# Optimization experiments

Hardware: AMD Instinct MI355X
Metric: run time of the kernel (lower is better)

## Reference

```python
import jax, jax.numpy as jnp
import numpy as np

M, K, N = 4096, 4096, 11008


def setup_inputs() -> dict:
    key = jax.random.key(0)
    k1, k2, k3 = jax.random.split(key, 3)
    x = jax.random.normal(k1, (M, K), dtype=jnp.float16)
    weight_packed = jax.random.randint(k2, ((K + 1) // 2, N), 0, 256, dtype=jnp.int32)
    weight_scale = jax.random.uniform(k3, (N,), dtype=jnp.float32) * 0.05 + 1e-3
    return {"x": x, "weight_packed": weight_packed, "weight_scale": weight_scale}


def reference(x, weight_packed, weight_scale):
    # Unpack int4 nibbles: low nibble -> even K index, high nibble -> odd K index.
    packed = weight_packed.astype(jnp.uint8)                      # [K//2, N]
    low = (packed & 15).astype(jnp.float32) - 8.0                 # even rows
    high = ((packed >> 4) & 15).astype(jnp.float32) - 8.0         # odd rows
    k = x.shape[-1]
    w = jnp.stack([low, high], axis=1).reshape(-1, low.shape[1])[:k]  # [K, N]
    # Per-output-feature symmetric scale, then fp16 GEMM (matches torch fallback).
    w = (w * weight_scale[None, :]).astype(jnp.float16)
    out = jnp.matmul(x, w)                                        # [M, N] fp16
    return out
```

## Files before the change

### kernel.cpp

```cpp
#include <hip/hip_runtime.h>
#include <hip/hip_fp16.h>
#include <stdint.h>


#define M_DIM 4096
#define K_DIM 4096
#define N_DIM 11008
#define KH    (K_DIM / 2)

#define WS_XH_BYTES  ((size_t)M_DIM * K_DIM * 2)

typedef __attribute__((ext_vector_type(8))) _Float16 f16x8;
typedef __attribute__((ext_vector_type(2))) _Float16 h2;
typedef __attribute__((ext_vector_type(4))) float f32x4;

__device__ __forceinline__ unsigned pack_f16_pair(float lo, float hi) {
    return __builtin_bit_cast(unsigned, __builtin_amdgcn_cvt_pkrtz(lo, hi));
}

__device__ __forceinline__ unsigned dq_pair(unsigned v) {
    unsigned c = (v & 0xFu) | ((v << 12) & 0x000F0000u) | 0x64006400u;
    h2 r = __builtin_bit_cast(h2, c) + __builtin_bit_cast(h2, 0xE408E408u);
    return __builtin_bit_cast(unsigned, r);
}

__device__ __forceinline__ void gld_lds16(const void* g, void* l) {
    __builtin_amdgcn_global_load_lds(
        (const __attribute__((address_space(1))) unsigned int*)g,
        (__attribute__((address_space(3))) unsigned int*)l,
        16, 0, 0);
}

__global__ void __launch_bounds__(256) cvt_x_kernel(
    const float* __restrict__ X, unsigned short* __restrict__ Xh)
{
    size_t i = ((size_t)blockIdx.x * 256 + threadIdx.x) * 8;
    float4 a = *(const float4*)(X + i);
    float4 b = *(const float4*)(X + i + 4);
    uint4 o = make_uint4(pack_f16_pair(a.x, a.y), pack_f16_pair(a.z, a.w),
                         pack_f16_pair(b.x, b.y), pack_f16_pair(b.z, b.w));
    *(uint4*)(Xh + i) = o;
}

__global__ void __launch_bounds__(256) dqt_kernel(
    const int* __restrict__ WP, unsigned* __restrict__ Wt)
{
    __shared__ unsigned Lt[64][65];
    const int t = threadIdx.x;
    const int n0 = blockIdx.x * 64;
    const int r0 = blockIdx.y * 64;
    const int g = t >> 6, l = t & 63;
#pragma unroll
    for (int i = 0; i < 16; ++i) {
        const int r = r0 + g * 16 + i;
        Lt[l][g * 16 + i] = dq_pair((unsigned)WP[(size_t)r * N_DIM + n0 + l]);
    }
    __syncthreads();
    const int nr = t >> 2, sg = t & 3;
    unsigned* dst = Wt + (size_t)(n0 + nr) * KH + r0 + sg * 16;
#pragma unroll
    for (int c = 0; c < 4; ++c) {
        uint4 v = make_uint4(Lt[nr][sg * 16 + c * 4 + 0], Lt[nr][sg * 16 + c * 4 + 1],
                             Lt[nr][sg * 16 + c * 4 + 2], Lt[nr][sg * 16 + c * 4 + 3]);
        *(uint4*)(dst + c * 4) = v;
    }
}

__global__ void __launch_bounds__(512, 2) qgemm9_kernel(
    const unsigned short* __restrict__ Xh,
    const unsigned*       __restrict__ Wt,
    const float*          __restrict__ WS,
    float*                __restrict__ Out)
{
    __shared__ unsigned short LA[2][2][8192];
    __shared__ unsigned short LB[2][2][8192];

    const int t = threadIdx.x;
    const int w = t >> 6;
    const int l = t & 63;

    const int bid = blockIdx.x;
    const int xcd = bid & 7;
    const int i8  = bid >> 3;
    const int bx  = i8 >> 1;
    const int by  = (xcd << 1) | (i8 & 1);
    const int bm0 = by * 256;
    const int bn0 = bx * 256;

    const int wr = w >> 2;
    const int wc = w & 3;

    f32x4 acc[8][4];
#pragma unroll
    for (int i = 0; i < 8; ++i)
#pragma unroll
        for (int j = 0; j < 4; ++j)
            acc[i][j] = (f32x4){0.f, 0.f, 0.f, 0.f};

    const int cS = (t & 7) ^ ((t >> 3) & 7);
    const unsigned short* gA = Xh + (size_t)(bm0 + (t >> 3)) * K_DIM + cS * 8;
    const unsigned*       gB = Wt + (size_t)(bn0 + (t >> 3)) * KH + cS * 4;
    const int t8 = t * 8;

#define SU_A(buf, h, c, kt)                                                   \
    gld_lds16(gA + (size_t)((h) * 128 + (c) * 64) * K_DIM + (size_t)(kt) * 64, \
              &LA[buf][h][(c) * 4096 + t8])
#define SU_B(buf, bh, ch, kt)                                                 \
    gld_lds16(gB + (size_t)((bh) * 128 + (ch) * 64) * KH + (size_t)(kt) * 32, \
              &LB[buf][bh][(ch) * 4096 + t8])

    const int lq = l >> 4;
    const int lr = l & 15;

    f16x8 af0[4][2], af1[4][2], bf0[2][2], bf1[2][2];

#define READ_AF(D, h, ARR) do {                                               \
    _Pragma("unroll")                                                         \
    for (int mi = 0; mi < 4; ++mi) {                                          \
        const int lrow = (h) * 64 + mi * 16 + lr;                             \
        _Pragma("unroll")                                                     \
        for (int ks = 0; ks < 2; ++ks)                                        \
            ARR[mi][ks] = *(const f16x8*)                                     \
                &LA[D][wr][lrow * 64 + (((ks * 4 + lq) ^ (lrow & 7)) * 8)];   \
    }                                                                         \
} while (0)

#define READ_BF(D, ch, ARR) do {                                              \
    _Pragma("unroll")                                                         \
    for (int n = 0; n < 2; ++n) {                                             \
        const int lrow = (wc & 1) * 64 + (ch) * 32 + n * 16 + lr;             \
        _Pragma("unroll")                                                     \
        for (int ks = 0; ks < 2; ++ks)                                        \
            ARR[n][ks] = *(const f16x8*)                                      \
                &LB[D][wc >> 1][lrow * 64 + (((ks * 4 + lq) ^ (lrow & 7)) * 8)]; \
    }                                                                         \
} while (0)

#define Q16(MB, AF, BF, NB) do {                                              \
    __builtin_amdgcn_s_setprio(1);                                            \
    _Pragma("unroll")                                                         \
    for (int ks = 0; ks < 2; ++ks)                                            \
        _Pragma("unroll")                                                     \
        for (int mi = 0; mi < 4; ++mi)                                        \
            _Pragma("unroll")                                                 \
            for (int n = 0; n < 2; ++n)                                       \
                acc[(MB) + mi][(NB) + n] =                                    \
                    __builtin_amdgcn_mfma_f32_16x16x32_f16(                   \
                        AF[mi][ks], BF[n][ks], acc[(MB) + mi][(NB) + n],      \
                        0, 0, 0);                                             \
    __builtin_amdgcn_s_setprio(0);                                            \
} while (0)

#define WAITV(n) asm volatile("s_waitcnt vmcnt(" #n ")" ::: "memory")
#define LGKM0()  do { asm volatile("s_waitcnt lgkmcnt(0)" ::: "memory");      \
                      __builtin_amdgcn_sched_barrier(0); } while (0)
#define BAR()    __builtin_amdgcn_s_barrier()

#define TILE_STD(D, DN, ktn) do {                                             \
    SU_B(DN, 0, 0, ktn); SU_B(DN, 0, 1, ktn);                                 \
    WAITV(4); BAR();                                                          \
    READ_AF(D, 0, af0); READ_BF(D, 0, bf0); LGKM0();                          \
    Q16(0, af0, bf0, 0);                                                      \
    SU_B(DN, 1, 0, ktn); SU_B(DN, 1, 1, ktn);                                 \
    READ_BF(D, 1, bf1); LGKM0();                                              \
    Q16(0, af0, bf1, 2);                                                      \
    SU_A(DN, 0, 0, ktn); SU_A(DN, 1, 0, ktn);                                 \
    WAITV(6); BAR();                                                          \
    READ_AF(D, 1, af1); LGKM0();                                              \
    Q16(4, af1, bf1, 2);                                                      \
    SU_A(DN, 0, 1, ktn); SU_A(DN, 1, 1, ktn);                                 \
    Q16(4, af1, bf0, 0);                                                      \
} while (0)

#define TILE_LAST(D) do {                                                     \
    WAITV(2); BAR();                                                          \
    READ_AF(D, 0, af0); READ_BF(D, 0, bf0); LGKM0();                          \
    Q16(0, af0, bf0, 0);                                                      \
    READ_BF(D, 1, bf1); LGKM0();                                              \
    Q16(0, af0, bf1, 2);                                                      \
    WAITV(0); BAR();                                                          \
    READ_AF(D, 1, af1); LGKM0();                                              \
    Q16(4, af1, bf1, 2);                                                      \
    Q16(4, af1, bf0, 0);                                                      \
} while (0)

    SU_B(0, 0, 0, 0); SU_B(0, 0, 1, 0); SU_B(0, 1, 0, 0); SU_B(0, 1, 1, 0);
    SU_A(0, 0, 0, 0); SU_A(0, 1, 0, 0); SU_A(0, 0, 1, 0); SU_A(0, 1, 1, 0);

    for (int i = 0; i < 31; ++i) {
        TILE_STD(0, 1, 2 * i + 1);
        TILE_STD(1, 0, 2 * i + 2);
    }
    TILE_STD(0, 1, 63);
    TILE_LAST(1);

#pragma unroll
    for (int ni = 0; ni < 4; ++ni) {
        const int col = bn0 + wc * 64 + ni * 16 + lr;
        const float s = WS[col];
#pragma unroll
        for (int mi = 0; mi < 8; ++mi) {
            const int row = bm0 + wr * 128 + mi * 16 + lq * 4;
#pragma unroll
            for (int i = 0; i < 4; ++i) {
                Out[(size_t)(row + i) * N_DIM + col] = acc[mi][ni][i] * s;
            }
        }
    }
#undef SU_A
#undef SU_B
#undef READ_AF
#undef READ_BF
#undef Q16
#undef WAITV
#undef LGKM0
#undef BAR
#undef TILE_STD
#undef TILE_LAST
}

extern "C" void kernel_launch(void* const* d_in, const int* in_sizes, int n_in,
                              void* d_out, int out_size, void* d_ws, size_t ws_size,
                              hipStream_t stream) {
    const float* X  = (const float*)d_in[0];
    const int*   WP = (const int*)d_in[1];
    const float* WS = (const float*)d_in[2];
    float*       Out = (float*)d_out;

    unsigned short* Xh = (unsigned short*)d_ws;
    unsigned*       Wt = (unsigned*)((char*)d_ws + WS_XH_BYTES);

    cvt_x_kernel<<<(M_DIM * K_DIM) / (256 * 8), 256, 0, stream>>>(X, Xh);
    dim3 gdq(N_DIM / 64, KH / 64);
    dqt_kernel<<<gdq, 256, 0, stream>>>(WP, Wt);
    dim3 grid((N_DIM / 256) * (M_DIM / 256));
    qgemm9_kernel<<<grid, 512, 0, stream>>>(Xh, Wt, WS, Out);
}
```

Measured before the change: 408.8 us.

## Switch GEMM inner loop from 16x16x32 to 32x32x16 MFMA tiles

```diff
diff --git a/kernel.cpp b/kernel.cpp
--- a/kernel.cpp
+++ b/kernel.cpp
@@ -10,9 +10,9 @@
 
 #define WS_XH_BYTES  ((size_t)M_DIM * K_DIM * 2)
 
-typedef __attribute__((ext_vector_type(8))) _Float16 f16x8;
-typedef __attribute__((ext_vector_type(2))) _Float16 h2;
-typedef __attribute__((ext_vector_type(4))) float f32x4;
+typedef __attribute__((ext_vector_type(8)))  _Float16 f16x8;
+typedef __attribute__((ext_vector_type(2)))  _Float16 h2;
+typedef __attribute__((ext_vector_type(16))) float f32x16;
 
 __device__ __forceinline__ unsigned pack_f16_pair(float lo, float hi) {
     return __builtin_bit_cast(unsigned, __builtin_amdgcn_cvt_pkrtz(lo, hi));
@@ -66,7 +66,7 @@
     }
 }
 
-__global__ void __launch_bounds__(512, 2) qgemm9_kernel(
+__global__ void __launch_bounds__(512, 2) qgemm10_kernel(
     const unsigned short* __restrict__ Xh,
     const unsigned*       __restrict__ Wt,
     const float*          __restrict__ WS,
@@ -90,12 +90,12 @@
     const int wr = w >> 2;
     const int wc = w & 3;
 
-    f32x4 acc[8][4];
-#pragma unroll
-    for (int i = 0; i < 8; ++i)
-#pragma unroll
-        for (int j = 0; j < 4; ++j)
-            acc[i][j] = (f32x4){0.f, 0.f, 0.f, 0.f};
+    f32x16 acc[4][2];
+#pragma unroll
+    for (int i = 0; i < 4; ++i)
+#pragma unroll
+        for (int j = 0; j < 2; ++j)
+            acc[i][j] = (f32x16)(0.0f);
 
     const int cS = (t & 7) ^ ((t >> 3) & 7);
     const unsigned short* gA = Xh + (size_t)(bm0 + (t >> 3)) * K_DIM + cS * 8;
@@ -109,45 +109,50 @@
     gld_lds16(gB + (size_t)((bh) * 128 + (ch) * 64) * KH + (size_t)(kt) * 32, \
               &LB[buf][bh][(ch) * 4096 + t8])
 
-    const int lq = l >> 4;
-    const int lr = l & 15;
-
-    f16x8 af0[4][2], af1[4][2], bf0[2][2], bf1[2][2];
-
-#define READ_AF(D, h, ARR) do {                                               \
-    _Pragma("unroll")                                                         \
-    for (int mi = 0; mi < 4; ++mi) {                                          \
-        const int lrow = (h) * 64 + mi * 16 + lr;                             \
-        _Pragma("unroll")                                                     \
-        for (int ks = 0; ks < 2; ++ks)                                        \
-            ARR[mi][ks] = *(const f16x8*)                                     \
-                &LA[D][wr][lrow * 64 + (((ks * 4 + lq) ^ (lrow & 7)) * 8)];   \
+    const int hi  = l >> 5;
+    const int sw0 = (hi ^ (l & 7)) * 16;
+    const int aoff = wr * 16384 + (l & 31) * 128 + sw0;
+    const int boff = (wc >> 1) * 16384 + ((wc & 1) * 64 + (l & 31)) * 128 + sw0;
+    const char* const baseA = (const char*)&LA[0][0][0];
+    const char* const baseB = (const char*)&LB[0][0][0];
+    const char* const pA[4] = { baseA + aoff, baseA + (aoff ^ 32),
+                                baseA + (aoff ^ 64), baseA + (aoff ^ 96) };
+    const char* const pB[4] = { baseB + boff, baseB + (boff ^ 32),
+                                baseB + (boff ^ 64), baseB + (boff ^ 96) };
+
+    f16x8 af01[2][4], af23[2][4], bf0[4], bf1[4];
+
+#define READ_AF01(D) do {                                                     \
+    _Pragma("unroll")                                                         \
+    for (int ks = 0; ks < 4; ++ks) {                                          \
+        af01[0][ks] = *(const f16x8*)(pA[ks] + ((D) * 32768 + 0 * 4096));     \
+        af01[1][ks] = *(const f16x8*)(pA[ks] + ((D) * 32768 + 1 * 4096));     \
     }                                                                         \
 } while (0)
 
-#define READ_BF(D, ch, ARR) do {                                              \
-    _Pragma("unroll")                                                         \
-    for (int n = 0; n < 2; ++n) {                                             \
-        const int lrow = (wc & 1) * 64 + (ch) * 32 + n * 16 + lr;             \
-        _Pragma("unroll")                                                     \
-        for (int ks = 0; ks < 2; ++ks)                                        \
-            ARR[n][ks] = *(const f16x8*)                                      \
-                &LB[D][wc >> 1][lrow * 64 + (((ks * 4 + lq) ^ (lrow & 7)) * 8)]; \
+#define READ_AF23(D) do {                                                     \
+    _Pragma("unroll")                                                         \
+    for (int ks = 0; ks < 4; ++ks) {                                          \
+        af23[0][ks] = *(const f16x8*)(pA[ks] + ((D) * 32768 + 2 * 4096));     \
+        af23[1][ks] = *(const f16x8*)(pA[ks] + ((D) * 32768 + 3 * 4096));     \
     }                                                                         \
 } while (0)
 
-#define Q16(MB, AF, BF, NB) do {                                              \
+#define READ_BF(D, nb, ARR) do {                                              \
+    _Pragma("unroll")                                                         \
+    for (int ks = 0; ks < 4; ++ks)                                            \
+        ARR[ks] = *(const f16x8*)(pB[ks] + ((D) * 32768 + (nb) * 4096));      \
+} while (0)
+
+#define Q8(AF, MB0, BF, NB) do {                                              \
     __builtin_amdgcn_s_setprio(1);                                            \
     _Pragma("unroll")                                                         \
-    for (int ks = 0; ks < 2; ++ks)                                            \
-        _Pragma("unroll")                                                     \
-        for (int mi = 0; mi < 4; ++mi)                                        \
-            _Pragma("unroll")                                                 \
-            for (int n = 0; n < 2; ++n)                                       \
-                acc[(MB) + mi][(NB) + n] =                                    \
-                    __builtin_amdgcn_mfma_f32_16x16x32_f16(                   \
-                        AF[mi][ks], BF[n][ks], acc[(MB) + mi][(NB) + n],      \
-                        0, 0, 0);                                             \
+    for (int ks = 0; ks < 4; ++ks) {                                          \
+        acc[(MB0) + 0][NB] = __builtin_amdgcn_mfma_f32_32x32x16_f16(          \
+            AF[0][ks], BF[ks], acc[(MB0) + 0][NB], 0, 0, 0);                  \
+        acc[(MB0) + 1][NB] = __builtin_amdgcn_mfma_f32_32x32x16_f16(          \
+            AF[1][ks], BF[ks], acc[(MB0) + 1][NB], 0, 0, 0);                  \
+    }                                                                         \
     __builtin_amdgcn_s_setprio(0);                                            \
 } while (0)
 
@@ -159,29 +164,29 @@
 #define TILE_STD(D, DN, ktn) do {                                             \
     SU_B(DN, 0, 0, ktn); SU_B(DN, 0, 1, ktn);                                 \
     WAITV(4); BAR();                                                          \
-    READ_AF(D, 0, af0); READ_BF(D, 0, bf0); LGKM0();                          \
-    Q16(0, af0, bf0, 0);                                                      \
+    READ_AF01(D); READ_BF(D, 0, bf0); LGKM0();                                \
+    Q8(af01, 0, bf0, 0);                                                      \
     SU_B(DN, 1, 0, ktn); SU_B(DN, 1, 1, ktn);                                 \
     READ_BF(D, 1, bf1); LGKM0();                                              \
-    Q16(0, af0, bf1, 2);                                                      \
+    Q8(af01, 0, bf1, 1);                                                      \
     SU_A(DN, 0, 0, ktn); SU_A(DN, 1, 0, ktn);                                 \
     WAITV(6); BAR();                                                          \
-    READ_AF(D, 1, af1); LGKM0();                                              \
-    Q16(4, af1, bf1, 2);                                                      \
+    READ_AF23(D); LGKM0();                                                    \
+    Q8(af23, 2, bf1, 1);                                                      \
     SU_A(DN, 0, 1, ktn); SU_A(DN, 1, 1, ktn);                                 \
-    Q16(4, af1, bf0, 0);                                                      \
+    Q8(af23, 2, bf0, 0);                                                      \
 } while (0)
 
 #define TILE_LAST(D) do {                                                     \
     WAITV(2); BAR();                                                          \
-    READ_AF(D, 0, af0); READ_BF(D, 0, bf0); LGKM0();                          \
-    Q16(0, af0, bf0, 0);                                                      \
+    READ_AF01(D); READ_BF(D, 0, bf0); LGKM0();                                \
+    Q8(af01, 0, bf0, 0);                                                      \
     READ_BF(D, 1, bf1); LGKM0();                                              \
-    Q16(0, af0, bf1, 2);                                                      \
+    Q8(af01, 0, bf1, 1);                                                      \
     WAITV(0); BAR();                                                          \
-    READ_AF(D, 1, af1); LGKM0();                                              \
-    Q16(4, af1, bf1, 2);                                                      \
-    Q16(4, af1, bf0, 0);                                                      \
+    READ_AF23(D); LGKM0();                                                    \
+    Q8(af23, 2, bf1, 1);                                                      \
+    Q8(af23, 2, bf0, 0);                                                      \
 } while (0)
 
     SU_B(0, 0, 0, 0); SU_B(0, 0, 1, 0); SU_B(0, 1, 0, 0); SU_B(0, 1, 1, 0);
@@ -195,23 +200,25 @@
     TILE_LAST(1);
 
 #pragma unroll
-    for (int ni = 0; ni < 4; ++ni) {
-        const int col = bn0 + wc * 64 + ni * 16 + lr;
+    for (int nb = 0; nb < 2; ++nb) {
+        const int col = bn0 + wc * 64 + nb * 32 + (l & 31);
         const float s = WS[col];
 #pragma unroll
-        for (int mi = 0; mi < 8; ++mi) {
-            const int row = bm0 + wr * 128 + mi * 16 + lq * 4;
-#pragma unroll
-            for (int i = 0; i < 4; ++i) {
-                Out[(size_t)(row + i) * N_DIM + col] = acc[mi][ni][i] * s;
+        for (int mb = 0; mb < 4; ++mb) {
+            const int rbase = bm0 + wr * 128 + mb * 32 + 4 * hi;
+#pragma unroll
+            for (int reg = 0; reg < 16; ++reg) {
+                const int row = rbase + (reg & 3) + 8 * (reg >> 2);
+                Out[(size_t)row * N_DIM + col] = acc[mb][nb][reg] * s;
             }
         }
     }
 #undef SU_A
 #undef SU_B
-#undef READ_AF
+#undef READ_AF01
+#undef READ_AF23
 #undef READ_BF
-#undef Q16
+#undef Q8
 #undef WAITV
 #undef LGKM0
 #undef BAR
@@ -234,5 +241,5 @@
     dim3 gdq(N_DIM / 64, KH / 64);
     dqt_kernel<<<gdq, 256, 0, stream>>>(WP, Wt);
     dim3 grid((N_DIM / 256) * (M_DIM / 256));
-    qgemm9_kernel<<<grid, 512, 0, stream>>>(Xh, Wt, WS, Out);
-}
+    qgemm10_kernel<<<grid, 512, 0, stream>>>(Xh, Wt, WS, Out);
+}
```

Result: no change. 415.7 us (+1.7%).

## Load B fragments directly from global into registers, double-buffered, dropping LDS for B

Applied to the files above, without the earlier changes.

```diff
diff --git a/kernel.cpp b/kernel.cpp
--- a/kernel.cpp
+++ b/kernel.cpp
@@ -66,14 +66,13 @@
     }
 }
 
-__global__ void __launch_bounds__(512, 2) qgemm9_kernel(
+__global__ void __launch_bounds__(512, 2) qgemm12_kernel(
     const unsigned short* __restrict__ Xh,
     const unsigned*       __restrict__ Wt,
     const float*          __restrict__ WS,
     float*                __restrict__ Out)
 {
     __shared__ unsigned short LA[2][2][8192];
-    __shared__ unsigned short LB[2][2][8192];
 
     const int t = threadIdx.x;
     const int w = t >> 6;
@@ -99,20 +98,38 @@
 
     const int cS = (t & 7) ^ ((t >> 3) & 7);
     const unsigned short* gA = Xh + (size_t)(bm0 + (t >> 3)) * K_DIM + cS * 8;
-    const unsigned*       gB = Wt + (size_t)(bn0 + (t >> 3)) * KH + cS * 4;
     const int t8 = t * 8;
 
 #define SU_A(buf, h, c, kt)                                                   \
     gld_lds16(gA + (size_t)((h) * 128 + (c) * 64) * K_DIM + (size_t)(kt) * 64, \
               &LA[buf][h][(c) * 4096 + t8])
-#define SU_B(buf, bh, ch, kt)                                                 \
-    gld_lds16(gB + (size_t)((bh) * 128 + (ch) * 64) * KH + (size_t)(kt) * 32, \
-              &LB[buf][bh][(ch) * 4096 + t8])
+#define STAGE_A4(buf, kt) do {                                                \
+    SU_A(buf, 0, 0, kt); SU_A(buf, 0, 1, kt);                                 \
+    SU_A(buf, 1, 0, kt); SU_A(buf, 1, 1, kt);                                 \
+} while (0)
 
     const int lq = l >> 4;
     const int lr = l & 15;
 
-    f16x8 af0[4][2], af1[4][2], bf0[2][2], bf1[2][2];
+    unsigned vo[4];
+#pragma unroll
+    for (int ni = 0; ni < 4; ++ni)
+        vo[ni] = (unsigned)(((wc * 64 + ni * 16 + lr) * KH + lq * 4) * 4);
+    const char* const bB = (const char*)(Wt + (size_t)bn0 * KH);
+
+    uint4 bfP[4][2], bfQ[4][2];
+
+#define LOAD_BF(SET, kt) do {                                                 \
+    const char* _b0 = bB + (size_t)(kt) * 128;                                \
+    const char* _b1 = _b0 + 64;                                               \
+    _Pragma("unroll")                                                         \
+    for (int ni = 0; ni < 4; ++ni) {                                          \
+        SET[ni][0] = *(const uint4*)(_b0 + vo[ni]);                           \
+        SET[ni][1] = *(const uint4*)(_b1 + vo[ni]);                           \
+    }                                                                         \
+} while (0)
+
+    f16x8 af0[4][2], af1[4][2];
 
 #define READ_AF(D, h, ARR) do {                                               \
     _Pragma("unroll")                                                         \
@@ -125,18 +142,7 @@
     }                                                                         \
 } while (0)
 
-#define READ_BF(D, ch, ARR) do {                                              \
-    _Pragma("unroll")                                                         \
-    for (int n = 0; n < 2; ++n) {                                             \
-        const int lrow = (wc & 1) * 64 + (ch) * 32 + n * 16 + lr;             \
-        _Pragma("unroll")                                                     \
-        for (int ks = 0; ks < 2; ++ks)                                        \
-            ARR[n][ks] = *(const f16x8*)                                      \
-                &LB[D][wc >> 1][lrow * 64 + (((ks * 4 + lq) ^ (lrow & 7)) * 8)]; \
-    }                                                                         \
-} while (0)
-
-#define Q16(MB, AF, BF, NB) do {                                              \
+#define Q16(MB, AF, SET, NB) do {                                             \
     __builtin_amdgcn_s_setprio(1);                                            \
     _Pragma("unroll")                                                         \
     for (int ks = 0; ks < 2; ++ks)                                            \
@@ -146,8 +152,9 @@
             for (int n = 0; n < 2; ++n)                                       \
                 acc[(MB) + mi][(NB) + n] =                                    \
                     __builtin_amdgcn_mfma_f32_16x16x32_f16(                   \
-                        AF[mi][ks], BF[n][ks], acc[(MB) + mi][(NB) + n],      \
-                        0, 0, 0);                                             \
+                        AF[mi][ks],                                           \
+                        __builtin_bit_cast(f16x8, SET[(NB) + n][ks]),         \
+                        acc[(MB) + mi][(NB) + n], 0, 0, 0);                   \
     __builtin_amdgcn_s_setprio(0);                                            \
 } while (0)
 
@@ -156,43 +163,54 @@
                       __builtin_amdgcn_sched_barrier(0); } while (0)
 #define BAR()    __builtin_amdgcn_s_barrier()
 
-#define TILE_STD(D, DN, ktn) do {                                             \
-    SU_B(DN, 0, 0, ktn); SU_B(DN, 0, 1, ktn);                                 \
-    WAITV(4); BAR();                                                          \
-    READ_AF(D, 0, af0); READ_BF(D, 0, bf0); LGKM0();                          \
-    Q16(0, af0, bf0, 0);                                                      \
-    SU_B(DN, 1, 0, ktn); SU_B(DN, 1, 1, ktn);                                 \
-    READ_BF(D, 1, bf1); LGKM0();                                              \
-    Q16(0, af0, bf1, 2);                                                      \
-    SU_A(DN, 0, 0, ktn); SU_A(DN, 1, 0, ktn);                                 \
-    WAITV(6); BAR();                                                          \
+#define TILE_STD(D, CUR, NXT, kt1, kt2) do {                                  \
+    WAITV(4);                             \
+    LOAD_BF(NXT, kt1);                           \
+    READ_AF(D, 0, af0); LGKM0();                                              \
+    Q16(0, af0, CUR, 0);                                                      \
+    Q16(0, af0, CUR, 2);                                                      \
     READ_AF(D, 1, af1); LGKM0();                                              \
-    Q16(4, af1, bf1, 2);                                                      \
-    SU_A(DN, 0, 1, ktn); SU_A(DN, 1, 1, ktn);                                 \
-    Q16(4, af1, bf0, 0);                                                      \
-} while (0)
-
-#define TILE_LAST(D) do {                                                     \
-    WAITV(2); BAR();                                                          \
-    READ_AF(D, 0, af0); READ_BF(D, 0, bf0); LGKM0();                          \
-    Q16(0, af0, bf0, 0);                                                      \
-    READ_BF(D, 1, bf1); LGKM0();                                              \
-    Q16(0, af0, bf1, 2);                                                      \
-    WAITV(0); BAR();                                                          \
+    Q16(4, af1, CUR, 2);                                                      \
+    Q16(4, af1, CUR, 0);                                                      \
+    WAITV(8);                           \
+    BAR();                                    \
+    STAGE_A4(D, kt2);                           \
+} while (0)
+
+#define TILE_62(D, CUR, NXT) do {                                             \
+    WAITV(4);                                                                 \
+    LOAD_BF(NXT, 63);                                                         \
+    READ_AF(D, 0, af0); LGKM0();                                              \
+    Q16(0, af0, CUR, 0);                                                      \
+    Q16(0, af0, CUR, 2);                                                      \
     READ_AF(D, 1, af1); LGKM0();                                              \
-    Q16(4, af1, bf1, 2);                                                      \
-    Q16(4, af1, bf0, 0);                                                      \
-} while (0)
-
-    SU_B(0, 0, 0, 0); SU_B(0, 0, 1, 0); SU_B(0, 1, 0, 0); SU_B(0, 1, 1, 0);
-    SU_A(0, 0, 0, 0); SU_A(0, 1, 0, 0); SU_A(0, 0, 1, 0); SU_A(0, 1, 1, 0);
+    Q16(4, af1, CUR, 2);                                                      \
+    Q16(4, af1, CUR, 0);                                                      \
+    WAITV(8); BAR();                                                          \
+} while (0)
+
+#define TILE_63(D, CUR) do {                                                  \
+    WAITV(0);                                              \
+    READ_AF(D, 0, af0); LGKM0();                                              \
+    Q16(0, af0, CUR, 0);                                                      \
+    Q16(0, af0, CUR, 2);                                                      \
+    READ_AF(D, 1, af1); LGKM0();                                              \
+    Q16(4, af1, CUR, 2);                                                      \
+    Q16(4, af1, CUR, 0);                                                      \
+} while (0)
+
+    STAGE_A4(0, 0);
+    LOAD_BF(bfP, 0);
+    STAGE_A4(1, 1);
+    WAITV(12);
+    BAR();
 
     for (int i = 0; i < 31; ++i) {
-        TILE_STD(0, 1, 2 * i + 1);
-        TILE_STD(1, 0, 2 * i + 2);
-    }
-    TILE_STD(0, 1, 63);
-    TILE_LAST(1);
+        TILE_STD(0, bfP, bfQ, 2 * i + 1, 2 * i + 2);
+        TILE_STD(1, bfQ, bfP, 2 * i + 2, 2 * i + 3);
+    }
+    TILE_62(0, bfP, bfQ);
+    TILE_63(1, bfQ);
 
 #pragma unroll
     for (int ni = 0; ni < 4; ++ni) {
@@ -208,15 +226,16 @@
         }
     }
 #undef SU_A
-#undef SU_B
+#undef STAGE_A4
+#undef LOAD_BF
 #undef READ_AF
-#undef READ_BF
 #undef Q16
 #undef WAITV
 #undef LGKM0
 #undef BAR
 #undef TILE_STD
-#undef TILE_LAST
+#undef TILE_62
+#undef TILE_63
 }
 
 extern "C" void kernel_launch(void* const* d_in, const int* in_sizes, int n_in,
@@ -234,5 +253,5 @@
     dim3 gdq(N_DIM / 64, KH / 64);
     dqt_kernel<<<gdq, 256, 0, stream>>>(WP, Wt);
     dim3 grid((N_DIM / 256) * (M_DIM / 256));
-    qgemm9_kernel<<<grid, 512, 0, stream>>>(Xh, Wt, WS, Out);
-}
+    qgemm12_kernel<<<grid, 512, 0, stream>>>(Xh, Wt, WS, Out);
+}
```

After: 565.0 us. 38.2% more time.
